# Kernel optimization log

Measured on AMD Instinct MI355X. Metric: run time of the kernel, lower is better.

The kernel has to match this reference:

```python
import jax, jax.numpy as jnp
import numpy as np

B, N, D = 512, 8, 2048
NP = N * (N - 1)  # number of ordered pairs


def _mlp2(h, w0, b0, w1, b1):
    # Linear -> ReLU -> Linear -> ReLU (matches Sequential with one extra layer)
    h = jax.nn.relu(h @ w0 + b0)
    return jax.nn.relu(h @ w1 + b1)


def setup_inputs() -> dict:
    key = jax.random.key(0)
    ks = jax.random.split(key, 10)
    s = 0.02
    x = jax.random.normal(ks[0], (B, N, D), dtype=jnp.float32)
    # structured pair index: for each object i, its N-1 neighbors j (j != i), col2 = valid flag
    pairs = np.array([(i, j, 1) for i in range(N) for j in range(N) if j != i], dtype=np.int32)
    g_idx = jnp.asarray(np.broadcast_to(pairs[None], (B, NP, 3)).copy())
    def w(k, shape):
        return jax.random.normal(k, shape, dtype=jnp.float32) * s
    return {
        "x": x, "g_idx": g_idx,
        "sd_w0": w(ks[1], (D, D)), "sd_b0": jnp.zeros((D,), jnp.float32),
        "sd_w1": w(ks[2], (D, D)), "sd_b1": jnp.zeros((D,), jnp.float32),
        "rd_w0": w(ks[3], (2 * D, D)), "rd_b0": jnp.zeros((D,), jnp.float32),
        "rd_w1": w(ks[4], (D, D)), "rd_b1": jnp.zeros((D,), jnp.float32),
        "af_w0": w(ks[5], (D, D)), "af_b0": jnp.zeros((D,), jnp.float32),
        "af_w1": w(ks[6], (D, D)), "af_b1": jnp.zeros((D,), jnp.float32),
        "ag_w0": w(ks[7], (2 * D, D)), "ag_b0": jnp.zeros((D,), jnp.float32),
        "ag_w1": w(ks[8], (D, D)), "ag_b1": jnp.zeros((D,), jnp.float32),
    }


def reference(x, g_idx, sd_w0, sd_b0, sd_w1, sd_b1, rd_w0, rd_b0, rd_w1, rd_b1,
              af_w0, af_b0, af_w1, af_b1, ag_w0, ag_b0, ag_w1, ag_b1):
    b, n, d = x.shape
    s = x
    # x1 = x.repeat(1, n-1, 1): row k of x1 equals x[:, k % n]
    x1 = jnp.tile(x, (1, n - 1, 1))                      # [B, N*(N-1), D]
    y1 = jnp.take_along_axis(x1, g_idx[..., 0:1], axis=1)  # [B, NP, D]
    y2 = jnp.take_along_axis(x1, g_idx[..., 1:2], axis=1)
    r = jnp.concatenate([y1, y2], axis=-1) * g_idx[:, :, 2:3].astype(x.dtype)  # [B, NP, 2D]
    r = r.reshape(b, n, n - 1, 2 * d)
    r = _mlp2(r, rd_w0, rd_b0, rd_w1, rd_b1)             # [B, N, N-1, D]
    r = r.sum(axis=2)                                    # [B, N, D]
    xs = _mlp2(x, sd_w0, sd_b0, sd_w1, sd_b1)            # [B, N, D]
    pred = xs + r
    a = _mlp2(pred, af_w0, af_b0, af_w1, af_b1)
    a = jnp.concatenate([a, s], axis=2)                  # [B, N, 2D]
    out = _mlp2(a, ag_w0, ag_b0, ag_w1, ag_b1)           # [B, N, D]
    return out
```

## Files before the change

kernel.cpp:

```cpp
#include <hip/hip_runtime.h>
#include <hip/hip_bf16.h>

typedef __bf16 bf16_t;
typedef __bf16 bf16x8 __attribute__((ext_vector_type(8)));
typedef float f32x4 __attribute__((ext_vector_type(4)));

#define DEVINL static __device__ __forceinline__

DEVINL void gload_lds16(const void* g, void* l) {
  __builtin_amdgcn_global_load_lds(
      (__attribute__((address_space(1))) void*)g,
      (__attribute__((address_space(3))) void*)l, 16, 0, 0);
}

__global__ __launch_bounds__(256) void k_cvt_bf16(const float* __restrict__ in,
                                                  bf16_t* __restrict__ out, int n8) {
  int t = blockIdx.x * 256 + threadIdx.x;
  if (t >= n8) return;
  const float4* p = (const float4*)in + (size_t)t * 2;
  float4 a = p[0], b = p[1];
  bf16x8 o;
  o[0] = (bf16_t)a.x; o[1] = (bf16_t)a.y; o[2] = (bf16_t)a.z; o[3] = (bf16_t)a.w;
  o[4] = (bf16_t)b.x; o[5] = (bf16_t)b.y; o[6] = (bf16_t)b.z; o[7] = (bf16_t)b.w;
  *(bf16x8*)(out + (size_t)t * 8) = o;
}

struct TP10 { const float* s[10]; bf16_t* d[10]; int ld[10]; };
__global__ __launch_bounds__(256) void k_transpose10(TP10 a) {
  __shared__ float tile[32][33];
  const int z = blockIdx.z;
  const float* W = a.s[z];
  bf16_t* WT = a.d[z];
  const int dld = a.ld[z];
  int tx = threadIdx.x & 31, ty = threadIdx.x >> 5;
  int n0 = blockIdx.x * 32, k0 = blockIdx.y * 32;
  #pragma unroll
  for (int i = 0; i < 32; i += 8)
    tile[ty + i][tx] = W[(size_t)(k0 + ty + i) * 2048 + n0 + tx];
  __syncthreads();
  #pragma unroll
  for (int i = 0; i < 32; i += 8)
    WT[(size_t)(n0 + ty + i) * dld + k0 + tx] = (bf16_t)tile[tx][ty + i];
}

__global__ __launch_bounds__(256) void k_h1(const bf16_t* __restrict__ uv, int ldu,
                                            int uo, int vo,
                                            const float* __restrict__ b0,
                                            bf16_t* __restrict__ h1, int pbase) {
  int pl = blockIdx.x;
  int c0 = threadIdx.x * 8;
  int p = pbase + pl;
  int b = p >> 6, q = p & 63;
  int i = q >> 3, jj = q & 7;
  if (jj == 7) {
    bf16x8 z = {};
    *(bf16x8*)(h1 + (size_t)pl * 2048 + c0) = z;
    return;
  }
  int j = jj + (jj >= i ? 1 : 0);
  bf16x8 u = *(const bf16x8*)(uv + (size_t)(b * 8 + i) * ldu + uo + c0);
  bf16x8 v = *(const bf16x8*)(uv + (size_t)(b * 8 + j) * ldu + vo + c0);
  const float4* bp = (const float4*)(b0 + c0);
  float4 ba = bp[0], bb4 = bp[1];
  float bb[8] = {ba.x, ba.y, ba.z, ba.w, bb4.x, bb4.y, bb4.z, bb4.w};
  bf16x8 h;
  #pragma unroll
  for (int e = 0; e < 8; ++e)
    h[e] = (bf16_t)fmaxf((float)u[e] + (float)v[e] + bb[e], 0.f);
  *(bf16x8*)(h1 + (size_t)pl * 2048 + c0) = h;
}

template <typename TOUT, int BM, int BN, int NW, int MODE>
__global__ __launch_bounds__(NW * 64, 2) void k_gemm(
    const bf16_t* __restrict__ A, const bf16_t* __restrict__ A2, int lda, int ksplit,
    const bf16_t* __restrict__ BT, int ldb,
    const float* __restrict__ bias, int act_ncol,
    TOUT* __restrict__ C, int N, int K,
    const bf16_t* __restrict__ xsp, int drow) {
  constexpr int WN = NW / 2;
  constexpr int MF = BM / 32;
  constexpr int MH = MF / 2;
  constexpr int NF = BN / (16 * WN);
  static_assert(NF == 4, "engine assumes 4 B-fragments per wave");
  constexpr int AQ = BM / (16 * NW);
  constexpr int BQ = BN / (16 * NW);
  constexpr int AHALF = BM * 64;
  constexpr int BHALF = BN * 64;
  constexpr int AREG = 2 * AHALF;
  constexpr int BUFS = AREG + 2 * BHALF;
  constexpr int NWAIT = AQ + 2 * BQ;

  extern __shared__ char smem[];
  const int t = threadIdx.x;
  const int w = t >> 6, l = t & 63;

  const int nwg = gridDim.x * gridDim.y;
  const int bid = blockIdx.y * gridDim.x + blockIdx.x;
  const int q8 = nwg >> 3, r8 = nwg & 7, xcd = bid & 7, sidx = bid >> 3;
  const int wg = (xcd < r8 ? xcd * (q8 + 1) : r8 * (q8 + 1) + (xcd - r8) * q8) + sidx;
  const int NB = gridDim.x;
  int mb, nb;
  if (((NB & 1) | (nwg & 3) | ((nwg / NB) & 1)) == 0) {
    int wg2 = wg >> 2, r2 = wg & 3, sc = NB >> 1;
    mb = (wg2 / sc) * 2 + (r2 >> 1);
    nb = (wg2 % sc) * 2 + (r2 & 1);
  } else {
    mb = wg / NB; nb = wg % NB;
  }
  const int m0 = mb * BM, n0 = nb * BN;

  size_t Aoffq[AQ], Boffq[BQ];
  #pragma unroll
  for (int q = 0; q < AQ; ++q) {
    int r = w * (BM / NW) + q * 16 + (l >> 2);
    int sq = (((l & 3) ^ ((r >> 1) & 3))) * 8;
    Aoffq[q] = (size_t)(m0 + r) * lda + sq;
  }
  #pragma unroll
  for (int q = 0; q < BQ; ++q) {
    int r = w * (BN / NW) + q * 16 + (l >> 2);
    int sq = (((l & 3) ^ ((r >> 1) & 3))) * 8;
    Boffq[q] = (size_t)(n0 + r) * ldb + sq;
  }
  const int nkt = K >> 6;

  auto stage = [&](int tau, int buf, int h) {
    const int isA = h & 1, kh = h >> 1;
    char* lb = smem + buf * BUFS + (isA ? kh * AHALF : AREG + kh * BHALF) +
               w * (isA ? (AHALF / NW) : (BHALF / NW));
    const int kk = tau * 64 + kh * 32;
    if (isA) {
      const bf16_t* Ab = A;
      int sub = 0;
      if (A2 != nullptr && tau * 64 >= ksplit) { Ab = A2; sub = ksplit; }
      #pragma unroll
      for (int q = 0; q < AQ; ++q)
        gload_lds16(Ab + Aoffq[q] + (kk - sub), lb + q * 1024);
    } else {
      #pragma unroll
      for (int q = 0; q < BQ; ++q)
        gload_lds16(BT + Boffq[q] + kk, lb + q * 1024);
    }
  };

  const int wm = w / WN, wn = w % WN;
  const int lr = l & 15, lg = l >> 4;
  int aoff[MF], boff[NF];
  #pragma unroll
  for (int mf = 0; mf < MF; ++mf) {
    int r = wm * (BM / 2) + mf * 16 + lr;
    aoff[mf] = r * 64 + ((lg ^ ((r >> 1) & 3)) << 4);
  }
  #pragma unroll
  for (int nf = 0; nf < NF; ++nf) {
    int r = wn * 64 + nf * 16 + lr;
    boff[nf] = AREG + r * 64 + ((lg ^ ((r >> 1) & 3)) << 4);
  }

  f32x4 acc[MF][NF] = {};

  #pragma unroll
  for (int h = 0; h < 4; ++h) stage(0, 0, h);
  {
    int t1 = nkt > 1 ? 1 : 0;
    stage(t1, 1, 0); stage(t1, 1, 1); stage(t1, 1, 2);
  }
  if constexpr (NWAIT == 6) asm volatile("s_waitcnt vmcnt(6)");
  else                      asm volatile("s_waitcnt vmcnt(5)");
  __builtin_amdgcn_sched_barrier(0);
  __builtin_amdgcn_s_barrier();

  auto tile_body = [&](int tile, int buf) {
    char* base = smem + buf * BUFS;
    const int tn1 = (tile + 1 < nkt) ? tile + 1 : nkt - 1;
    const int tn2 = (tile + 2 < nkt) ? tile + 2 : nkt - 1;
    bf16x8 af[MH], bfr[NF];

    #pragma unroll
    for (int nf = 0; nf < NF; ++nf) bfr[nf] = *(const bf16x8*)(base + boff[nf]);
    #pragma unroll
    for (int mf = 0; mf < MH; ++mf) af[mf] = *(const bf16x8*)(base + aoff[mf]);
    stage(tn1, buf ^ 1, 3);
    __builtin_amdgcn_s_setprio(1);
    #pragma unroll
    for (int mf = 0; mf < MH; ++mf)
      #pragma unroll
      for (int nf = 0; nf < NF; ++nf)
        acc[mf][nf] = __builtin_amdgcn_mfma_f32_16x16x32_bf16(af[mf], bfr[nf], acc[mf][nf], 0, 0, 0);
    __builtin_amdgcn_s_setprio(0);
    __builtin_amdgcn_sched_barrier(0);
    __builtin_amdgcn_s_barrier();

    #pragma unroll
    for (int mf = 0; mf < MH; ++mf) af[mf] = *(const bf16x8*)(base + aoff[MH + mf]);
    stage(tn2, buf, 0);
    __builtin_amdgcn_s_setprio(1);
    #pragma unroll
    for (int mf = 0; mf < MH; ++mf)
      #pragma unroll
      for (int nf = 0; nf < NF; ++nf)
        acc[MH + mf][nf] = __builtin_amdgcn_mfma_f32_16x16x32_bf16(af[mf], bfr[nf], acc[MH + mf][nf], 0, 0, 0);
    __builtin_amdgcn_s_setprio(0);
    __builtin_amdgcn_sched_barrier(0);
    __builtin_amdgcn_s_barrier();

    #pragma unroll
    for (int nf = 0; nf < NF; ++nf) bfr[nf] = *(const bf16x8*)(base + BHALF + boff[nf]);
    #pragma unroll
    for (int mf = 0; mf < MH; ++mf) af[mf] = *(const bf16x8*)(base + AHALF + aoff[mf]);
    stage(tn2, buf, 1);
    __builtin_amdgcn_s_setprio(1);
    #pragma unroll
    for (int mf = 0; mf < MH; ++mf)
      #pragma unroll
      for (int nf = 0; nf < NF; ++nf)
        acc[mf][nf] = __builtin_amdgcn_mfma_f32_16x16x32_bf16(af[mf], bfr[nf], acc[mf][nf], 0, 0, 0);
    __builtin_amdgcn_s_setprio(0);
    __builtin_amdgcn_sched_barrier(0);
    __builtin_amdgcn_s_barrier();

    #pragma unroll
    for (int mf = 0; mf < MH; ++mf) af[mf] = *(const bf16x8*)(base + AHALF + aoff[MH + mf]);
    stage(tn2, buf, 2);
    __builtin_amdgcn_s_setprio(1);
    #pragma unroll
    for (int mf = 0; mf < MH; ++mf)
      #pragma unroll
      for (int nf = 0; nf < NF; ++nf)
        acc[MH + mf][nf] = __builtin_amdgcn_mfma_f32_16x16x32_bf16(af[mf], bfr[nf], acc[MH + mf][nf], 0, 0, 0);
    __builtin_amdgcn_s_setprio(0);
    __builtin_amdgcn_sched_barrier(0);
    if constexpr (NWAIT == 6) asm volatile("s_waitcnt vmcnt(6)");
    else                      asm volatile("s_waitcnt vmcnt(5)");
    __builtin_amdgcn_s_barrier();
  };

  for (int tt = 0; tt < nkt; tt += 2) {
    tile_body(tt, 0);
    tile_body(tt + 1, 1);
  }
  asm volatile("s_waitcnt vmcnt(0)");

  if constexpr (MODE == 1) {
    const int g = lg >> 1;
    const bool hi = (lg & 1) != 0;
    #pragma unroll
    for (int mf = 0; mf < MF; ++mf) {
      #pragma unroll
      for (int nf = 0; nf < NF; ++nf) {
        int col = n0 + wn * 64 + nf * 16 + lr;
        float bv = bias[col];
        float s = fmaxf(acc[mf][nf][0] + bv, 0.f) +
                  fmaxf(acc[mf][nf][1] + bv, 0.f) +
                  fmaxf(acc[mf][nf][2] + bv, 0.f);
        if (!hi) s += fmaxf(acc[mf][nf][3] + bv, 0.f);
        s += __shfl_xor(s, 16, 64);
        if (!hi) {
          int d = drow + (m0 >> 3) + wm * (BM >> 4) + mf * 2 + g;
          float xv = (float)xsp[(size_t)d * N + col];
          C[(size_t)d * N + col] = (TOUT)(xv + s);
        }
      }
    }
  } else {
    #pragma unroll
    for (int mf = 0; mf < MF; ++mf) {
      #pragma unroll
      for (int nf = 0; nf < NF; ++nf) {
        int col = n0 + wn * 64 + nf * 16 + lr;
        bool act = col < act_ncol;
        float bv = act ? bias[col] : 0.f;
        #pragma unroll
        for (int ri = 0; ri < 4; ++ri) {
          int row = m0 + wm * (BM / 2) + mf * 16 + lg * 4 + ri;
          float v = acc[mf][nf][ri] + bv;
          if (act) v = fmaxf(v, 0.f);
          C[(size_t)row * N + col] = (TOUT)v;
        }
      }
    }
  }
}

extern "C" void kernel_launch(void* const* d_in, const int* in_sizes, int n_in,
                              void* d_out, int out_size, void* d_ws, size_t ws_size,
                              hipStream_t stream) {
  const float* x     = (const float*)d_in[0];
  const float* sd_w0 = (const float*)d_in[2];
  const float* sd_b0 = (const float*)d_in[3];
  const float* sd_w1 = (const float*)d_in[4];
  const float* sd_b1 = (const float*)d_in[5];
  const float* rd_w0 = (const float*)d_in[6];
  const float* rd_b0 = (const float*)d_in[7];
  const float* rd_w1 = (const float*)d_in[8];
  const float* rd_b1 = (const float*)d_in[9];
  const float* af_w0 = (const float*)d_in[10];
  const float* af_b0 = (const float*)d_in[11];
  const float* af_w1 = (const float*)d_in[12];
  const float* af_b1 = (const float*)d_in[13];
  const float* ag_w0 = (const float*)d_in[14];
  const float* ag_b0 = (const float*)d_in[15];
  const float* ag_w1 = (const float*)d_in[16];
  const float* ag_b1 = (const float*)d_in[17];
  float* out = (float*)d_out;

  const int D = 2048, M = 4096;
  const size_t DD = (size_t)D * D;
  const size_t MN = (size_t)M * D;
  const int MCP = 16384;
  const size_t LDS256 = 131072, LDS128 = 98304;

  hipFuncSetAttribute((const void*)k_gemm<bf16_t, 256, 256, 8, 0>,
                      hipFuncAttributeMaxDynamicSharedMemorySize, (int)LDS256);
  hipFuncSetAttribute((const void*)k_gemm<bf16_t, 256, 256, 8, 1>,
                      hipFuncAttributeMaxDynamicSharedMemorySize, (int)LDS256);
  hipFuncSetAttribute((const void*)k_gemm<bf16_t, 128, 256, 8, 0>,
                      hipFuncAttributeMaxDynamicSharedMemorySize, (int)LDS256);
  hipFuncSetAttribute((const void*)k_gemm<float, 128, 256, 8, 0>,
                      hipFuncAttributeMaxDynamicSharedMemorySize, (int)LDS256);

  char* wp = (char*)d_ws;
  auto alloc = [&](size_t bytes) -> void* {
    void* p = (void*)wp;
    wp += (bytes + 255) & ~(size_t)255;
    return p;
  };
  bf16_t* xb    = (bf16_t*)alloc(MN * 2);
  bf16_t* wcat  = (bf16_t*)alloc((size_t)3 * DD * 2);
  bf16_t* sdw1T = (bf16_t*)alloc(DD * 2);
  bf16_t* rdw1T = (bf16_t*)alloc(DD * 2);
  bf16_t* afw0T = (bf16_t*)alloc(DD * 2);
  bf16_t* afw1T = (bf16_t*)alloc(DD * 2);
  bf16_t* agw0T = (bf16_t*)alloc(DD * 4);
  bf16_t* agw1T = (bf16_t*)alloc(DD * 2);
  bf16_t* tuv   = (bf16_t*)alloc(MN * 3 * 2);
  bf16_t* xs    = (bf16_t*)alloc(MN * 2);
  bf16_t* h1c   = (bf16_t*)alloc((size_t)MCP * D * 2);
  bf16_t* predb = (bf16_t*)alloc(MN * 2);
  (void)ws_size; (void)in_sizes; (void)n_in; (void)out_size;

  bf16_t* S1 = h1c;
  bf16_t* S2 = h1c + MN;

  k_cvt_bf16<<<dim3(M * D / 8 / 256), 256, 0, stream>>>(x, xb, M * D / 8);

  TP10 tp;
  tp.s[0] = sd_w0;           tp.d[0] = wcat;            tp.ld[0] = D;
  tp.s[1] = rd_w0;           tp.d[1] = wcat + DD;       tp.ld[1] = D;
  tp.s[2] = rd_w0 + DD;      tp.d[2] = wcat + 2 * DD;   tp.ld[2] = D;
  tp.s[3] = sd_w1;           tp.d[3] = sdw1T;           tp.ld[3] = D;
  tp.s[4] = rd_w1;           tp.d[4] = rdw1T;           tp.ld[4] = D;
  tp.s[5] = af_w0;           tp.d[5] = afw0T;           tp.ld[5] = D;
  tp.s[6] = af_w1;           tp.d[6] = afw1T;           tp.ld[6] = D;
  tp.s[7] = ag_w1;           tp.d[7] = agw1T;           tp.ld[7] = D;
  tp.s[8] = ag_w0;           tp.d[8] = agw0T;           tp.ld[8] = 2 * D;
  tp.s[9] = ag_w0 + DD;      tp.d[9] = agw0T + D;       tp.ld[9] = 2 * D;
  k_transpose10<<<dim3(64, 64, 10), 256, 0, stream>>>(tp);

  dim3 g128(D / 256, M / 128);

  k_gemm<bf16_t, 256, 256, 8, 0><<<dim3(24, 16), 512, LDS256, stream>>>(
      xb, nullptr, D, 0, wcat, D, sd_b0, D, tuv, 3 * D, D, nullptr, 0);
  k_gemm<bf16_t, 128, 256, 8, 0><<<g128, 512, LDS128, stream>>>(
      tuv, nullptr, 3 * D, 0, sdw1T, D, sd_b1, D, xs, D, D, nullptr, 0);

  for (int c = 0; c < 2; ++c) {
    k_h1<<<dim3(MCP), 256, 0, stream>>>(tuv, 3 * D, D, 2 * D, rd_b0, h1c, c * MCP);
    k_gemm<bf16_t, 256, 256, 8, 1><<<dim3(D / 256, MCP / 256), 512, LDS256, stream>>>(
        h1c, nullptr, D, 0, rdw1T, D, rd_b1, D, predb, D, D, xs, c * 2048);
  }

  k_gemm<bf16_t, 128, 256, 8, 0><<<g128, 512, LDS128, stream>>>(
      predb, nullptr, D, 0, afw0T, D, af_b0, D, S1, D, D, nullptr, 0);
  k_gemm<bf16_t, 128, 256, 8, 0><<<g128, 512, LDS128, stream>>>(
      S1, nullptr, D, 0, afw1T, D, af_b1, D, S2, D, D, nullptr, 0);
  k_gemm<bf16_t, 128, 256, 8, 0><<<g128, 512, LDS128, stream>>>(
      S2, xb, D, D, agw0T, 2 * D, ag_b0, D, S1, D, 2 * D, nullptr, 0);
  k_gemm<float, 128, 256, 8, 0><<<g128, 512, LDS128, stream>>>(
      S1, nullptr, D, 0, agw1T, D, ag_b1, D, out, D, D, nullptr, 0);
}
```

Before: 698.5 us.

## Merge prep kernels, retile first GEMM, and run pair stage unchunked when workspace allows

Folds the x-to-bf16 conversion into the weight-transpose kernel as an extra grid slice, which saves one launch. Switches the first concatenated-weight GEMM from 256x256 to 128x256 tiles, doubling its block count to 768 for better CU occupancy. When the workspace is large enough, the pair hidden stage and its GEMM run once over all 32768 rows instead of in two chunks. This removes launches and improves wave fill in the large GEMM, at the cost of twice the h1 buffer memory.

```diff
diff --git a/kernel.cpp b/kernel.cpp
--- a/kernel.cpp
+++ b/kernel.cpp
@@ -13,20 +13,18 @@
       (__attribute__((address_space(3))) void*)l, 16, 0, 0);
 }
 
-__global__ __launch_bounds__(256) void k_cvt_bf16(const float* __restrict__ in,
-                                                  bf16_t* __restrict__ out, int n8) {
-  int t = blockIdx.x * 256 + threadIdx.x;
-  if (t >= n8) return;
-  const float4* p = (const float4*)in + (size_t)t * 2;
-  float4 a = p[0], b = p[1];
-  bf16x8 o;
-  o[0] = (bf16_t)a.x; o[1] = (bf16_t)a.y; o[2] = (bf16_t)a.z; o[3] = (bf16_t)a.w;
-  o[4] = (bf16_t)b.x; o[5] = (bf16_t)b.y; o[6] = (bf16_t)b.z; o[7] = (bf16_t)b.w;
-  *(bf16x8*)(out + (size_t)t * 8) = o;
-}
-
-struct TP10 { const float* s[10]; bf16_t* d[10]; int ld[10]; };
-__global__ __launch_bounds__(256) void k_transpose10(TP10 a) {
+struct Prep { const float* s[10]; bf16_t* d[10]; int ld[10]; const float* x; bf16_t* xb; };
+__global__ __launch_bounds__(256) void k_prep(Prep a) {
+  if (blockIdx.z == 10) {
+    int t = (blockIdx.y * 64 + blockIdx.x) * 256 + threadIdx.x;
+    const float4* p = (const float4*)a.x + (size_t)t * 2;
+    float4 u = p[0], v = p[1];
+    bf16x8 o;
+    o[0] = (bf16_t)u.x; o[1] = (bf16_t)u.y; o[2] = (bf16_t)u.z; o[3] = (bf16_t)u.w;
+    o[4] = (bf16_t)v.x; o[5] = (bf16_t)v.y; o[6] = (bf16_t)v.z; o[7] = (bf16_t)v.w;
+    *(bf16x8*)(a.xb + (size_t)t * 8) = o;
+    return;
+  }
   __shared__ float tile[32][33];
   const int z = blockIdx.z;
   const float* W = a.s[z];
@@ -310,8 +308,6 @@
   const int MCP = 16384;
   const size_t LDS256 = 131072, LDS128 = 98304;
 
-  hipFuncSetAttribute((const void*)k_gemm<bf16_t, 256, 256, 8, 0>,
-                      hipFuncAttributeMaxDynamicSharedMemorySize, (int)LDS256);
   hipFuncSetAttribute((const void*)k_gemm<bf16_t, 256, 256, 8, 1>,
                       hipFuncAttributeMaxDynamicSharedMemorySize, (int)LDS256);
   hipFuncSetAttribute((const void*)k_gemm<bf16_t, 128, 256, 8, 0>,
@@ -335,16 +331,18 @@
   bf16_t* agw1T = (bf16_t*)alloc(DD * 2);
   bf16_t* tuv   = (bf16_t*)alloc(MN * 3 * 2);
   bf16_t* xs    = (bf16_t*)alloc(MN * 2);
-  bf16_t* h1c   = (bf16_t*)alloc((size_t)MCP * D * 2);
+  const size_t used0 = (size_t)(wp - (char*)d_ws);
+  const size_t h1big = (size_t)2 * MCP * D * 2;
+  const size_t h1sm  = (size_t)MCP * D * 2;
+  const bool big = ws_size >= used0 + h1big + MN * 2 + 1024;
+  bf16_t* h1c   = (bf16_t*)alloc(big ? h1big : h1sm);
   bf16_t* predb = (bf16_t*)alloc(MN * 2);
-  (void)ws_size; (void)in_sizes; (void)n_in; (void)out_size;
+  (void)in_sizes; (void)n_in; (void)out_size;
 
   bf16_t* S1 = h1c;
   bf16_t* S2 = h1c + MN;
 
-  k_cvt_bf16<<<dim3(M * D / 8 / 256), 256, 0, stream>>>(x, xb, M * D / 8);
-
-  TP10 tp;
+  Prep tp;
   tp.s[0] = sd_w0;           tp.d[0] = wcat;            tp.ld[0] = D;
   tp.s[1] = rd_w0;           tp.d[1] = wcat + DD;       tp.ld[1] = D;
   tp.s[2] = rd_w0 + DD;      tp.d[2] = wcat + 2 * DD;   tp.ld[2] = D;
@@ -355,19 +353,26 @@
   tp.s[7] = ag_w1;           tp.d[7] = agw1T;           tp.ld[7] = D;
   tp.s[8] = ag_w0;           tp.d[8] = agw0T;           tp.ld[8] = 2 * D;
   tp.s[9] = ag_w0 + DD;      tp.d[9] = agw0T + D;       tp.ld[9] = 2 * D;
-  k_transpose10<<<dim3(64, 64, 10), 256, 0, stream>>>(tp);
+  tp.x = x; tp.xb = xb;
+  k_prep<<<dim3(64, 64, 11), 256, 0, stream>>>(tp);
 
   dim3 g128(D / 256, M / 128);
 
-  k_gemm<bf16_t, 256, 256, 8, 0><<<dim3(24, 16), 512, LDS256, stream>>>(
+  k_gemm<bf16_t, 128, 256, 8, 0><<<dim3(24, 32), 512, LDS128, stream>>>(
       xb, nullptr, D, 0, wcat, D, sd_b0, D, tuv, 3 * D, D, nullptr, 0);
   k_gemm<bf16_t, 128, 256, 8, 0><<<g128, 512, LDS128, stream>>>(
       tuv, nullptr, 3 * D, 0, sdw1T, D, sd_b1, D, xs, D, D, nullptr, 0);
 
-  for (int c = 0; c < 2; ++c) {
-    k_h1<<<dim3(MCP), 256, 0, stream>>>(tuv, 3 * D, D, 2 * D, rd_b0, h1c, c * MCP);
-    k_gemm<bf16_t, 256, 256, 8, 1><<<dim3(D / 256, MCP / 256), 512, LDS256, stream>>>(
-        h1c, nullptr, D, 0, rdw1T, D, rd_b1, D, predb, D, D, xs, c * 2048);
+  if (big) {
+    k_h1<<<dim3(2 * MCP), 256, 0, stream>>>(tuv, 3 * D, D, 2 * D, rd_b0, h1c, 0);
+    k_gemm<bf16_t, 256, 256, 8, 1><<<dim3(D / 256, 2 * MCP / 256), 512, LDS256, stream>>>(
+        h1c, nullptr, D, 0, rdw1T, D, rd_b1, D, predb, D, D, xs, 0);
+  } else {
+    for (int c = 0; c < 2; ++c) {
+      k_h1<<<dim3(MCP), 256, 0, stream>>>(tuv, 3 * D, D, 2 * D, rd_b0, h1c, c * MCP);
+      k_gemm<bf16_t, 256, 256, 8, 1><<<dim3(D / 256, MCP / 256), 512, LDS256, stream>>>(
+          h1c, nullptr, D, 0, rdw1T, D, rd_b1, D, predb, D, D, xs, c * 2048);
+    }
   }
 
   k_gemm<bf16_t, 128, 256, 8, 0><<<g128, 512, LDS128, stream>>>(
```

After: 698.6 us. About the same (+0.0%).
